# Kernel optimization log

Measured on AMD Instinct MI355X. Metric: run time of the kernel, lower is better.

The kernel has to match this reference:

```python
import jax, jax.numpy as jnp
import numpy as np

COS_MARGIN = 0.35
ARC_MARGIN = 0.5
SCALE = 30.0
EPS = 1e-12

B, V = 2048, 32000


def setup_inputs() -> dict:
    key = jax.random.key(0)
    k1, k2 = jax.random.split(key)
    # logits are cosine similarities in [-1, 1]
    preds = jax.random.uniform(k1, (B, V), dtype=jnp.float32) * 2.0 - 1.0
    labels = jax.random.randint(k2, (B,), 0, V, dtype=jnp.int64)
    return {"preds": preds, "labels": labels}


def reference(preds, labels):
    # target cosine: preds[i, labels[i]]  (torch.diagonal(preds.T[labels]))
    target = jnp.take_along_axis(preds, labels[:, None], axis=1)[:, 0]
    theta = jnp.arccos(jnp.clip(target, -1.0 + EPS, 1.0 - EPS))
    theta = jnp.clip(theta, EPS, jnp.pi - EPS)  # 4*arctan(1) == pi
    numerator = SCALE * (jnp.cos(theta + ARC_MARGIN) - COS_MARGIN)  # [B]
    # sum of exp(scale * preds) over all classes except the target class
    cols = jnp.arange(preds.shape[1])  # [V]
    exp_all = jnp.exp(SCALE * preds)  # [B, V]
    sum_others = jnp.sum(jnp.where(cols[None, :] == labels[:, None], 0.0, exp_all), axis=1)
    denominator = jnp.exp(numerator) + sum_others
    return -jnp.mean(numerator - jnp.log(denominator))
```

## Files before the change

kernel.cpp:

```cpp
#include <hip/hip_runtime.h>
#include <math.h>

#define B_ROWS 2048
#define V_COLS 32000
#define SCALE_D 30.0
#define COS_MARGIN_D 0.35
#define ARC_MARGIN_D 0.5
#define EPS_D 1e-12
#define PI_D 3.14159265358979323846

#define LOG2E_X30 43.2808512266689022212f

typedef float f32x4 __attribute__((ext_vector_type(4)));


#define TPB_A 256
#define CHUNKS 4
#define V4_CHUNK (V_COLS / 4 / CHUNKS)
#define TAIL_T (V4_CHUNK - 7 * TPB_A)

#define EXP30(x) __builtin_amdgcn_exp2f((x) * LOG2E_X30)

__global__ __launch_bounds__(TPB_A, 8) void cosarc_partial_kernel(
    const float* __restrict__ preds,
    const int*   __restrict__ labels,
    double*      __restrict__ partials,
    float*       __restrict__ tgts)
{
    const int bid   = blockIdx.x;
    const int row   = bid >> 2;
    const int chunk = bid & 3;
    const int tid   = threadIdx.x;

    const float* rowp = preds + (size_t)row * V_COLS;
    const f32x4* p4   = (const f32x4*)rowp + chunk * V4_CHUNK;

    f32x4 v0 = p4[tid];
    f32x4 v1 = p4[tid + 1 * TPB_A];
    f32x4 v2 = p4[tid + 2 * TPB_A];
    f32x4 v3 = p4[tid + 3 * TPB_A];
    f32x4 v4 = p4[tid + 4 * TPB_A];
    f32x4 v5 = p4[tid + 5 * TPB_A];
    f32x4 v6 = p4[tid + 6 * TPB_A];
    const bool has8 = (tid < TAIL_T);
    f32x4 v7 = {0.f, 0.f, 0.f, 0.f};
    if (has8) v7 = p4[tid + 7 * TPB_A];

    if (tid == 0) {
        const int l  = labels[row];
        const int c0 = chunk * (V_COLS / CHUNKS);
        if (l >= c0 && l < c0 + (V_COLS / CHUNKS)) tgts[row] = rowp[l];
    }

    float sx, sy, sz, sw;
    sx  = EXP30(v0.x); sy  = EXP30(v0.y); sz  = EXP30(v0.z); sw  = EXP30(v0.w);
    sx += EXP30(v1.x); sy += EXP30(v1.y); sz += EXP30(v1.z); sw += EXP30(v1.w);
    sx += EXP30(v2.x); sy += EXP30(v2.y); sz += EXP30(v2.z); sw += EXP30(v2.w);
    sx += EXP30(v3.x); sy += EXP30(v3.y); sz += EXP30(v3.z); sw += EXP30(v3.w);
    sx += EXP30(v4.x); sy += EXP30(v4.y); sz += EXP30(v4.z); sw += EXP30(v4.w);
    sx += EXP30(v5.x); sy += EXP30(v5.y); sz += EXP30(v5.z); sw += EXP30(v5.w);
    sx += EXP30(v6.x); sy += EXP30(v6.y); sz += EXP30(v6.z); sw += EXP30(v6.w);
    if (has8) {
        sx += EXP30(v7.x); sy += EXP30(v7.y); sz += EXP30(v7.z); sw += EXP30(v7.w);
    }

    double sum = (double)((sx + sy) + (sz + sw));

    #pragma unroll
    for (int off = 32; off > 0; off >>= 1)
        sum += __shfl_down(sum, off, 64);

    __shared__ double wave_sums[TPB_A / 64];
    const int wave = tid >> 6;
    const int lane = tid & 63;
    if (lane == 0) wave_sums[wave] = sum;
    __syncthreads();

    if (tid == 0) {
        double total = 0.0;
        #pragma unroll
        for (int w = 0; w < TPB_A / 64; ++w) total += wave_sums[w];
        partials[bid] = total;
    }
}

__global__ __launch_bounds__(1024) void cosarc_final_kernel(
    const double* __restrict__ partials,
    const float*  __restrict__ tgts,
    float*        __restrict__ out)
{
    const int tid = threadIdx.x;
    double acc = 0.0;

    for (int r = tid; r < B_ROWS; r += 1024) {
        const double total = (partials[4 * r] + partials[4 * r + 1]) +
                             (partials[4 * r + 2] + partials[4 * r + 3]);
        const float tgt_f = tgts[r];
        const double sum_others = total - (double)EXP30(tgt_f);

        double t = (double)tgt_f;
        t = fmin(fmax(t, -1.0 + EPS_D), 1.0 - EPS_D);
        double theta = acos(t);
        theta = fmin(fmax(theta, EPS_D), PI_D - EPS_D);
        const double numerator = SCALE_D * (cos(theta + ARC_MARGIN_D) - COS_MARGIN_D);
        const double denominator = exp(numerator) + sum_others;
        acc += numerator - log(denominator);
    }

    #pragma unroll
    for (int off = 32; off > 0; off >>= 1)
        acc += __shfl_down(acc, off, 64);

    __shared__ double wave_sums[16];
    if ((tid & 63) == 0) wave_sums[tid >> 6] = acc;
    __syncthreads();

    if (tid == 0) {
        double total = 0.0;
        #pragma unroll
        for (int w = 0; w < 16; ++w) total += wave_sums[w];
        out[0] = (float)(-(total / (double)B_ROWS));
    }
}

extern "C" void kernel_launch(void* const* d_in, const int* in_sizes, int n_in,
                              void* d_out, int out_size, void* d_ws, size_t ws_size,
                              hipStream_t stream)
{
    const float* preds  = (const float*)d_in[0];
    const int*   labels = (const int*)d_in[1];
    float*       out    = (float*)d_out;

    double* partials = (double*)d_ws;
    float*  tgts     = (float*)((char*)d_ws + B_ROWS * CHUNKS * sizeof(double));

    cosarc_partial_kernel<<<B_ROWS * CHUNKS, TPB_A, 0, stream>>>(preds, labels, partials, tgts);
    cosarc_final_kernel<<<1, 1024, 0, stream>>>(partials, tgts, out);
}
```

Before: 352.0 us.

## Replace per-row chunk blocks with a flat grid-stride sweep and atomic row sums

The fixed 4-blocks-per-row partial kernel becomes a persistent grid of 2048 blocks that walks the whole matrix as a flat array. Each iteration prefetches the next vector with a nontemporal load. Each wave reduces its exp sums and atomically adds them as doubles into per-row accumulators, with handling for waves that straddle a row boundary. The final kernel now gathers the target logits itself. This trades many short-lived blocks for fewer long-lived ones, but it leaves each thread with only one outstanding load, adds many global double atomics and adds an extra memset launch.

```diff
diff --git a/kernel.cpp b/kernel.cpp
--- a/kernel.cpp
+++ b/kernel.cpp
@@ -13,90 +13,86 @@
 
 typedef float f32x4 __attribute__((ext_vector_type(4)));
 
-
-#define TPB_A 256
-#define CHUNKS 4
-#define V4_CHUNK (V_COLS / 4 / CHUNKS)
-#define TAIL_T (V4_CHUNK - 7 * TPB_A)
+#define TPB 256
+#define GRID 2048
+#define NV4_TOTAL (B_ROWS * (V_COLS / 4))
+#define NCHUNK (NV4_TOTAL / TPB)
 
 #define EXP30(x) __builtin_amdgcn_exp2f((x) * LOG2E_X30)
 
-__global__ __launch_bounds__(TPB_A, 8) void cosarc_partial_kernel(
+__global__ __launch_bounds__(TPB) void cosarc_sweep_kernel(
     const float* __restrict__ preds,
-    const int*   __restrict__ labels,
-    double*      __restrict__ partials,
-    float*       __restrict__ tgts)
+    double*      __restrict__ rowsum)
 {
-    const int bid   = blockIdx.x;
-    const int row   = bid >> 2;
-    const int chunk = bid & 3;
-    const int tid   = threadIdx.x;
+    const int b   = blockIdx.x;
+    const int tid = threadIdx.x;
+    const f32x4* p4 = (const f32x4*)preds;
 
-    const float* rowp = preds + (size_t)row * V_COLS;
-    const f32x4* p4   = (const f32x4*)rowp + chunk * V4_CHUNK;
+    int c = b;
+    f32x4 cur = __builtin_nontemporal_load(&p4[(size_t)c * TPB + tid]);
 
-    f32x4 v0 = p4[tid];
-    f32x4 v1 = p4[tid + 1 * TPB_A];
-    f32x4 v2 = p4[tid + 2 * TPB_A];
-    f32x4 v3 = p4[tid + 3 * TPB_A];
-    f32x4 v4 = p4[tid + 4 * TPB_A];
-    f32x4 v5 = p4[tid + 5 * TPB_A];
-    f32x4 v6 = p4[tid + 6 * TPB_A];
-    const bool has8 = (tid < TAIL_T);
-    f32x4 v7 = {0.f, 0.f, 0.f, 0.f};
-    if (has8) v7 = p4[tid + 7 * TPB_A];
+    for (int cn = c + GRID; ; cn += GRID) {
+        const bool more = (cn < NCHUNK);
+        f32x4 nxt = {0.f, 0.f, 0.f, 0.f};
+        if (more) nxt = __builtin_nontemporal_load(&p4[(size_t)cn * TPB + tid]);
 
-    if (tid == 0) {
-        const int l  = labels[row];
-        const int c0 = chunk * (V_COLS / CHUNKS);
-        if (l >= c0 && l < c0 + (V_COLS / CHUNKS)) tgts[row] = rowp[l];
-    }
+        {
+            const int base_f = c * (TPB * 4) + tid * 4;
+            const int wave_f = c * (TPB * 4) + (tid & ~63) * 4;
+            const int r0 = wave_f / V_COLS;
+            const int rA = base_f / V_COLS;
+            const int k  = min(4, V_COLS * (rA + 1) - base_f);
 
-    float sx, sy, sz, sw;
-    sx  = EXP30(v0.x); sy  = EXP30(v0.y); sz  = EXP30(v0.z); sw  = EXP30(v0.w);
-    sx += EXP30(v1.x); sy += EXP30(v1.y); sz += EXP30(v1.z); sw += EXP30(v1.w);
-    sx += EXP30(v2.x); sy += EXP30(v2.y); sz += EXP30(v2.z); sw += EXP30(v2.w);
-    sx += EXP30(v3.x); sy += EXP30(v3.y); sz += EXP30(v3.z); sw += EXP30(v3.w);
-    sx += EXP30(v4.x); sy += EXP30(v4.y); sz += EXP30(v4.z); sw += EXP30(v4.w);
-    sx += EXP30(v5.x); sy += EXP30(v5.y); sz += EXP30(v5.z); sw += EXP30(v5.w);
-    sx += EXP30(v6.x); sy += EXP30(v6.y); sz += EXP30(v6.z); sw += EXP30(v6.w);
-    if (has8) {
-        sx += EXP30(v7.x); sy += EXP30(v7.y); sz += EXP30(v7.z); sw += EXP30(v7.w);
-    }
+            const float e0 = EXP30(cur.x);
+            const float e1 = EXP30(cur.y);
+            const float e2 = EXP30(cur.z);
+            const float e3 = EXP30(cur.w);
 
-    double sum = (double)((sx + sy) + (sz + sw));
+            float sA = e0;
+            sA += (k > 1) ? e1 : 0.f;
+            sA += (k > 2) ? e2 : 0.f;
+            sA += (k > 3) ? e3 : 0.f;
+            const float sB = ((k <= 1) ? e1 : 0.f) +
+                             ((k <= 2) ? e2 : 0.f) +
+                             ((k <= 3) ? e3 : 0.f);
 
-    #pragma unroll
-    for (int off = 32; off > 0; off >>= 1)
-        sum += __shfl_down(sum, off, 64);
+            float clo = (rA == r0) ? sA : 0.f;
+            float chi = (rA == r0) ? sB : sA;
 
-    __shared__ double wave_sums[TPB_A / 64];
-    const int wave = tid >> 6;
-    const int lane = tid & 63;
-    if (lane == 0) wave_sums[wave] = sum;
-    __syncthreads();
+            const bool span = ((wave_f + 64 * 4 - 1) / V_COLS) != r0;
 
-    if (tid == 0) {
-        double total = 0.0;
-        #pragma unroll
-        for (int w = 0; w < TPB_A / 64; ++w) total += wave_sums[w];
-        partials[bid] = total;
+            #pragma unroll
+            for (int off = 32; off > 0; off >>= 1)
+                clo += __shfl_down(clo, off, 64);
+            if (span) {
+                #pragma unroll
+                for (int off = 32; off > 0; off >>= 1)
+                    chi += __shfl_down(chi, off, 64);
+            }
+            if ((tid & 63) == 0) {
+                atomicAdd(&rowsum[r0], (double)clo);
+                if (span) atomicAdd(&rowsum[r0 + 1], (double)chi);
+            }
+        }
+
+        if (!more) break;
+        cur = nxt;
+        c = cn;
     }
 }
 
 __global__ __launch_bounds__(1024) void cosarc_final_kernel(
-    const double* __restrict__ partials,
-    const float*  __restrict__ tgts,
+    const float*  __restrict__ preds,
+    const int*    __restrict__ labels,
+    const double* __restrict__ rowsum,
     float*        __restrict__ out)
 {
     const int tid = threadIdx.x;
     double acc = 0.0;
 
     for (int r = tid; r < B_ROWS; r += 1024) {
-        const double total = (partials[4 * r] + partials[4 * r + 1]) +
-                             (partials[4 * r + 2] + partials[4 * r + 3]);
-        const float tgt_f = tgts[r];
-        const double sum_others = total - (double)EXP30(tgt_f);
+        const float tgt_f = preds[(size_t)r * V_COLS + labels[r]];
+        const double sum_others = rowsum[r] - (double)EXP30(tgt_f);
 
         double t = (double)tgt_f;
         t = fmin(fmax(t, -1.0 + EPS_D), 1.0 - EPS_D);
@@ -130,10 +126,10 @@
     const float* preds  = (const float*)d_in[0];
     const int*   labels = (const int*)d_in[1];
     float*       out    = (float*)d_out;
+    double*      rowsum = (double*)d_ws;
 
-    double* partials = (double*)d_ws;
-    float*  tgts     = (float*)((char*)d_ws + B_ROWS * CHUNKS * sizeof(double));
+    hipMemsetAsync(rowsum, 0, B_ROWS * sizeof(double), stream);
 
-    cosarc_partial_kernel<<<B_ROWS * CHUNKS, TPB_A, 0, stream>>>(preds, labels, partials, tgts);
-    cosarc_final_kernel<<<1, 1024, 0, stream>>>(partials, tgts, out);
+    cosarc_sweep_kernel<<<GRID, TPB, 0, stream>>>(preds, rowsum);
+    cosarc_final_kernel<<<1, 1024, 0, stream>>>(preds, labels, rowsum, out);
 }
```

Measured after the change: 377.4 us. 1.07x slower.
